# Kernel optimization log

Hardware: AMD Instinct MI355X
Metric: run time of the kernel (lower is better)

The kernel has to match this reference:

```python
import jax, jax.numpy as jnp
import numpy as np

B, L, D = 1, 2048, 4096
H, KV, HD = 32, 8, 128
ROT = 64  # head_dim * partial_rotary_factor
SCALE = HD ** -0.5
NEG = -1e9


def _apply_rope(x, cos, sin):
    # x: [B, h, L, HD]; rotate only the first ROT dims (partial rotary, rotate-half convention)
    xr, xp = x[..., :ROT], x[..., ROT:]
    x1, x2 = jnp.split(xr, 2, axis=-1)
    rotated = jnp.concatenate([-x2, x1], axis=-1)
    xr = xr * cos[None, None] + rotated * sin[None, None]
    return jnp.concatenate([xr, xp], axis=-1)


def setup_inputs() -> dict:
    key = jax.random.key(0)
    k1, k2, k3 = jax.random.split(key, 3)
    x = jax.random.normal(k1, (B, L, D), jnp.float32)
    w_qkv = jax.random.normal(k2, (D, H * HD + 2 * KV * HD), jnp.float32) * 0.02
    w_o = jax.random.normal(k3, (H * HD, D), jnp.float32) * 0.02
    # causal additive mask, broadcast over batch and heads
    causal = jnp.tril(jnp.ones((L, L), dtype=bool))
    attention_mask = jnp.where(causal, 0.0, NEG).astype(jnp.float32)[None, None]
    # rotary tables over the ROT rotary dims
    inv_freq = 1.0 / (10000.0 ** (jnp.arange(0, ROT, 2, dtype=jnp.float32) / ROT))
    t = jnp.arange(L, dtype=jnp.float32)
    freqs = jnp.outer(t, inv_freq)            # [L, ROT/2]
    emb = jnp.concatenate([freqs, freqs], -1)  # [L, ROT]
    cos, sin = jnp.cos(emb), jnp.sin(emb)
    return {"x": x, "attention_mask": attention_mask, "cos": cos, "sin": sin,
            "w_qkv": w_qkv, "w_o": w_o}


def reference(x, attention_mask, cos, sin, w_qkv, w_o):
    Bx, Lx, _ = x.shape
    qkv = x @ w_qkv                                   # [B, L, H*HD + 2*KV*HD]
    q_pos = H * HD
    kv_pos = q_pos + KV * HD
    q = qkv[:, :, :q_pos].reshape(Bx, Lx, H, HD).transpose(0, 2, 1, 3)
    k = qkv[:, :, q_pos:kv_pos].reshape(Bx, Lx, KV, HD).transpose(0, 2, 1, 3)
    v = qkv[:, :, kv_pos:].reshape(Bx, Lx, KV, HD).transpose(0, 2, 1, 3)
    q = _apply_rope(q, cos, sin)
    k = _apply_rope(k, cos, sin)
    # GQA: duplicate KV heads (as in the original module)
    n_rep = H // KV
    k = jnp.repeat(k, n_rep, axis=1)
    v = jnp.repeat(v, n_rep, axis=1)
    w = jnp.einsum("bhqd,bhkd->bhqk", q, k) * SCALE   # [B, H, L, L]
    w = jax.nn.softmax(w + attention_mask, axis=-1)
    o = jnp.einsum("bhqk,bhkd->bhqd", w, v)           # [B, H, L, HD]
    o = o.transpose(0, 2, 1, 3).reshape(Bx, Lx, H * HD)
    return o @ w_o
```

## Files before the change

kernel.cpp:

```cpp
#include <hip/hip_runtime.h>
#include <stdint.h>

typedef float f32x4 __attribute__((ext_vector_type(4)));
typedef short s16x8 __attribute__((ext_vector_type(8)));
typedef unsigned short u16x4 __attribute__((ext_vector_type(4)));
typedef unsigned short u16x8 __attribute__((ext_vector_type(8)));

#define SCALE_F 0.08838834764831845f

__device__ __forceinline__ unsigned short f32_to_bf16(float f) {
    union { float f; unsigned int u; } v; v.f = f;
    return (unsigned short)((v.u + 0x7FFFu + ((v.u >> 16) & 1u)) >> 16);
}
__device__ __forceinline__ float bf16_to_f32(unsigned short h) {
    union { unsigned int u; float f; } v; v.u = (unsigned int)h << 16;
    return v.f;
}

__device__ __forceinline__ void gload16(const void* g, void* l) {
    __builtin_amdgcn_global_load_lds((const __attribute__((address_space(1))) unsigned int*)g,
                                     (__attribute__((address_space(3))) unsigned int*)l,
                                     16, 0, 0);
}

__global__ void k_conv_bf16(const float* __restrict__ in, unsigned short* __restrict__ out, int n4) {
    int i = blockIdx.x * 256 + threadIdx.x;
    if (i >= n4) return;
    f32x4 v = ((const f32x4*)in)[i];
    u16x4 o;
    o[0] = f32_to_bf16(v[0]); o[1] = f32_to_bf16(v[1]);
    o[2] = f32_to_bf16(v[2]); o[3] = f32_to_bf16(v[3]);
    ((u16x4*)out)[i] = o;
}

__global__ void k_transpose_f32(const float* __restrict__ in, unsigned short* __restrict__ out,
                                int R, int in_ld, int in_off) {
    __shared__ float tile[64][65];
    const int rb = blockIdx.y * 64, cb = blockIdx.x * 64;
    const int t = threadIdx.x;
    const int lr = t >> 4, lc4 = (t & 15) * 4;
#pragma unroll
    for (int i = 0; i < 4; ++i) {
        int r = i * 16 + lr;
        f32x4 v = *(const f32x4*)(in + (size_t)(rb + r) * in_ld + in_off + cb + lc4);
        tile[r][lc4 + 0] = v[0]; tile[r][lc4 + 1] = v[1];
        tile[r][lc4 + 2] = v[2]; tile[r][lc4 + 3] = v[3];
    }
    __syncthreads();
#pragma unroll
    for (int i = 0; i < 4; ++i) {
        int oc = cb + i * 16 + lr;
        u16x4 o;
#pragma unroll
        for (int j = 0; j < 4; ++j)
            o[j] = f32_to_bf16(tile[lc4 + j][i * 16 + lr]);
        *(u16x4*)(out + (size_t)oc * R + rb + lc4) = o;
    }
}

__global__ void k_transpose_b16(const unsigned short* __restrict__ in, unsigned short* __restrict__ out,
                                int R, int in_ld, int in_off) {
    __shared__ unsigned short tile[64][68];
    const int rb = blockIdx.y * 64, cb = blockIdx.x * 64;
    const int t = threadIdx.x;
    const int lr = t >> 4, lc4 = (t & 15) * 4;
#pragma unroll
    for (int i = 0; i < 4; ++i) {
        int r = i * 16 + lr;
        u16x4 v = *(const u16x4*)(in + (size_t)(rb + r) * in_ld + in_off + cb + lc4);
        tile[r][lc4 + 0] = v[0]; tile[r][lc4 + 1] = v[1];
        tile[r][lc4 + 2] = v[2]; tile[r][lc4 + 3] = v[3];
    }
    __syncthreads();
#pragma unroll
    for (int i = 0; i < 4; ++i) {
        int oc = cb + i * 16 + lr;
        u16x4 o;
#pragma unroll
        for (int j = 0; j < 4; ++j)
            o[j] = tile[lc4 + j][i * 16 + lr];
        *(u16x4*)(out + (size_t)oc * R + rb + lc4) = o;
    }
}

template<int BN, typename OUT>
__global__ __launch_bounds__(512, 1)
void k_gemm8p(const unsigned short* __restrict__ A, const unsigned short* __restrict__ Bt,
              OUT* __restrict__ C, int N, int K) {
    constexpr int BH = BN * 32;
    constexpr int NF = BN / 64;
    __shared__ __align__(16) unsigned short As[2][2][8192];
    __shared__ __align__(16) unsigned short Bs[2][2][BH];
    const int tid = threadIdx.x;
    const int lane = tid & 63, wid = tid >> 6;
    const int g = lane >> 4, l15 = lane & 15;
    const int wm = wid >> 2, wn = wid & 3;
    const int nwg = gridDim.x, bid = blockIdx.x;
    const int swz = (bid & 7) * (nwg >> 3) + (bid >> 3);
    const int ntn = N / BN;
    const int bm = swz / ntn, bn = swz - bm * ntn;
    const int brow = bm << 8, bcol = bn * BN;

    const int rS = tid >> 2;
    const int kcS = (tid & 3) ^ (rS & 3) ^ ((rS >> 2) & 3);
    const unsigned short* sA = A + (size_t)(brow + rS) * K + kcS * 8;
    const unsigned short* sB = Bt + (size_t)(bcol + rS) * K + kcS * 8;
    const int fsw = (g ^ (l15 & 3) ^ ((l15 >> 2) & 3)) * 8;

    f32x4 acc[8][NF] = {};
    const int nt = K >> 6;

    auto stA = [&](int t, int kh) {
        unsigned short* d = &As[t & 1][kh][tid * 8];
        const unsigned short* s = sA + (size_t)t * 64 + kh * 32;
        gload16(s, d);
        gload16(s + (size_t)128 * K, d + 4096);
    };
    auto stB = [&](int t, int kh) {
        unsigned short* d = &Bs[t & 1][kh][tid * 8];
        const unsigned short* s = sB + (size_t)t * 64 + kh * 32;
        gload16(s, d);
        if constexpr (BN == 256) gload16(s + (size_t)128 * K, d + 4096);
    };

    stA(0, 0); stB(0, 0); stA(0, 1); stB(0, 1);

    for (int t = 0; t < nt; ++t) {
        const int c = t & 1;
        if constexpr (BN == 256) {
            s16x8 af[4], bf[4];
            if (t + 1 < nt) { stA(t + 1, 0); asm volatile("s_waitcnt vmcnt(6)" ::: "memory"); }
            else            { asm volatile("s_waitcnt vmcnt(4)" ::: "memory"); }
            __builtin_amdgcn_s_barrier();
#pragma unroll
            for (int f = 0; f < 4; ++f)
                af[f] = *(const s16x8*)(&As[c][0][(wm * 128 + f * 16 + l15) * 32 + fsw]);
#pragma unroll
            for (int j = 0; j < 4; ++j)
                bf[j] = *(const s16x8*)(&Bs[c][0][(wn * 64 + j * 16 + l15) * 32 + fsw]);
            __builtin_amdgcn_s_setprio(1);
#pragma unroll
            for (int f = 0; f < 4; ++f)
#pragma unroll
                for (int j = 0; j < 4; ++j)
                    acc[f][j] = __builtin_amdgcn_mfma_f32_16x16x32_bf16(af[f], bf[j], acc[f][j], 0, 0, 0);
            __builtin_amdgcn_s_setprio(0);
            if (t + 1 < nt) stB(t + 1, 0);
#pragma unroll
            for (int f = 0; f < 4; ++f)
                af[f] = *(const s16x8*)(&As[c][0][(wm * 128 + 64 + f * 16 + l15) * 32 + fsw]);
            __builtin_amdgcn_s_setprio(1);
#pragma unroll
            for (int f = 0; f < 4; ++f)
#pragma unroll
                for (int j = 0; j < 4; ++j)
                    acc[4 + f][j] = __builtin_amdgcn_mfma_f32_16x16x32_bf16(af[f], bf[j], acc[4 + f][j], 0, 0, 0);
            __builtin_amdgcn_s_setprio(0);
            if (t + 1 < nt) { stA(t + 1, 1); asm volatile("s_waitcnt vmcnt(4)" ::: "memory"); }
            else            { asm volatile("s_waitcnt vmcnt(0)" ::: "memory"); }
            __builtin_amdgcn_s_barrier();
#pragma unroll
            for (int f = 0; f < 4; ++f)
                af[f] = *(const s16x8*)(&As[c][1][(wm * 128 + f * 16 + l15) * 32 + fsw]);
#pragma unroll
            for (int j = 0; j < 4; ++j)
                bf[j] = *(const s16x8*)(&Bs[c][1][(wn * 64 + j * 16 + l15) * 32 + fsw]);
            __builtin_amdgcn_s_setprio(1);
#pragma unroll
            for (int f = 0; f < 4; ++f)
#pragma unroll
                for (int j = 0; j < 4; ++j)
                    acc[f][j] = __builtin_amdgcn_mfma_f32_16x16x32_bf16(af[f], bf[j], acc[f][j], 0, 0, 0);
            __builtin_amdgcn_s_setprio(0);
            if (t + 1 < nt) stB(t + 1, 1);
#pragma unroll
            for (int f = 0; f < 4; ++f)
                af[f] = *(const s16x8*)(&As[c][1][(wm * 128 + 64 + f * 16 + l15) * 32 + fsw]);
            __builtin_amdgcn_s_setprio(1);
#pragma unroll
            for (int f = 0; f < 4; ++f)
#pragma unroll
                for (int j = 0; j < 4; ++j)
                    acc[4 + f][j] = __builtin_amdgcn_mfma_f32_16x16x32_bf16(af[f], bf[j], acc[4 + f][j], 0, 0, 0);
            __builtin_amdgcn_s_setprio(0);
        } else {
            s16x8 af[8], bf[2];
            if (t + 1 < nt) { stA(t + 1, 0); stB(t + 1, 0); asm volatile("s_waitcnt vmcnt(6)" ::: "memory"); }
            else            { asm volatile("s_waitcnt vmcnt(3)" ::: "memory"); }
            __builtin_amdgcn_s_barrier();
#pragma unroll
            for (int f = 0; f < 8; ++f)
                af[f] = *(const s16x8*)(&As[c][0][(wm * 128 + f * 16 + l15) * 32 + fsw]);
#pragma unroll
            for (int j = 0; j < 2; ++j)
                bf[j] = *(const s16x8*)(&Bs[c][0][(wn * 32 + j * 16 + l15) * 32 + fsw]);
            __builtin_amdgcn_s_setprio(1);
#pragma unroll
            for (int f = 0; f < 8; ++f)
#pragma unroll
                for (int j = 0; j < 2; ++j)
                    acc[f][j] = __builtin_amdgcn_mfma_f32_16x16x32_bf16(af[f], bf[j], acc[f][j], 0, 0, 0);
            __builtin_amdgcn_s_setprio(0);
            if (t + 1 < nt) { stA(t + 1, 1); stB(t + 1, 1); asm volatile("s_waitcnt vmcnt(6)" ::: "memory"); }
            else            { asm volatile("s_waitcnt vmcnt(0)" ::: "memory"); }
            __builtin_amdgcn_s_barrier();
#pragma unroll
            for (int f = 0; f < 8; ++f)
                af[f] = *(const s16x8*)(&As[c][1][(wm * 128 + f * 16 + l15) * 32 + fsw]);
#pragma unroll
            for (int j = 0; j < 2; ++j)
                bf[j] = *(const s16x8*)(&Bs[c][1][(wn * 32 + j * 16 + l15) * 32 + fsw]);
            __builtin_amdgcn_s_setprio(1);
#pragma unroll
            for (int f = 0; f < 8; ++f)
#pragma unroll
                for (int j = 0; j < 2; ++j)
                    acc[f][j] = __builtin_amdgcn_mfma_f32_16x16x32_bf16(af[f], bf[j], acc[f][j], 0, 0, 0);
            __builtin_amdgcn_s_setprio(0);
        }
    }

#pragma unroll
    for (int f = 0; f < 8; ++f)
#pragma unroll
        for (int j = 0; j < NF; ++j)
#pragma unroll
            for (int r = 0; r < 4; ++r) {
                const size_t idx = (size_t)(brow + wm * 128 + f * 16 + g * 4 + r) * N
                                   + bcol + wn * (BN / 4) + j * 16 + l15;
                if constexpr (sizeof(OUT) == 4) C[idx] = acc[f][j][r];
                else                            C[idx] = f32_to_bf16(acc[f][j][r]);
            }
}

__global__ void k_rope_pack(const unsigned short* __restrict__ qkv, const float* __restrict__ cosT,
                            const float* __restrict__ sinT, unsigned short* __restrict__ Qb,
                            unsigned short* __restrict__ Kb) {
    const int oct = blockIdx.x * 128 + threadIdx.x;
    if (oct >= 640) return;
    const int col = oct * 8;
    const int t = blockIdx.y;
    const int d = col & 127;
    u16x8 v8 = *(const u16x8*)(qkv + (size_t)t * 6144 + col);
    u16x8 o8;
    if (d < 64) {
        u16x8 p8 = *(const u16x8*)(qkv + (size_t)t * 6144 + (col ^ 32));
        f32x4 c0 = *(const f32x4*)(cosT + t * 64 + d);
        f32x4 c1 = *(const f32x4*)(cosT + t * 64 + d + 4);
        f32x4 s0 = *(const f32x4*)(sinT + t * 64 + d);
        f32x4 s1 = *(const f32x4*)(sinT + t * 64 + d + 4);
        const float sgn = (d < 32) ? -1.f : 1.f;
#pragma unroll
        for (int j = 0; j < 8; ++j) {
            float cc = (j < 4) ? c0[j] : c1[j - 4];
            float ss = (j < 4) ? s0[j] : s1[j - 4];
            float o = bf16_to_f32(v8[j]) * cc + sgn * bf16_to_f32(p8[j]) * ss;
            o8[j] = f32_to_bf16(o);
        }
    } else {
        o8 = v8;
    }
    if (col < 4096) {
        const int h = col >> 7;
        *(u16x8*)(Qb + ((size_t)h * 2048 + t) * 128 + d) = o8;
    } else {
        const int hk = (col - 4096) >> 7;
        *(u16x8*)(Kb + ((size_t)hk * 2048 + t) * 128 + d) = o8;
    }
}

__global__ __launch_bounds__(256, 2)
void k_attn(const unsigned short* __restrict__ Qb, const unsigned short* __restrict__ Kb,
            const unsigned short* __restrict__ Vt, unsigned short* __restrict__ Ob) {
    __shared__ __align__(16) unsigned short Ks[2][8192];
    __shared__ __align__(16) unsigned short Vs[2][8192];
    __shared__ __align__(16) unsigned short Pl[2][4][1024];
    const int h = blockIdx.y, hk = h >> 2;
    const int qbA = blockIdx.x, qbB = 31 - qbA;
    const int tid = threadIdx.x, lane = tid & 63, wid = tid >> 6;
    const int g = lane >> 4, l15 = lane & 15;
    const int qrA = qbA * 64 + wid * 16, qrB = qbB * 64 + wid * 16;
    const int swz = (l15 & 7) << 4;

    s16x8 aqA[4], aqB[4];
#pragma unroll
    for (int kc = 0; kc < 4; ++kc) {
        aqA[kc] = *(const s16x8*)(Qb + ((size_t)h * 2048 + qrA + l15) * 128 + kc * 32 + g * 8);
        aqB[kc] = *(const s16x8*)(Qb + ((size_t)h * 2048 + qrB + l15) * 128 + kc * 32 + g * 8);
    }

    const unsigned short* gK = Kb + ((size_t)hk * 2048 + (tid & 63)) * 128 + (tid >> 6) * 8;
    const unsigned short* gV = Vt + ((size_t)hk * 128 + (tid & 127)) * 2048 + (tid >> 7) * 8;

    auto stage = [&](int kb) {
        unsigned short* dK = Ks[kb & 1] + tid * 8;
        unsigned short* dV = Vs[kb & 1] + tid * 8;
        const unsigned short* sK = gK + (size_t)kb * 8192;
        const unsigned short* sV = gV + kb * 64;
#pragma unroll
        for (int i = 0; i < 4; ++i) gload16(sK + i * 32, dK + i * 2048);
#pragma unroll
        for (int i = 0; i < 4; ++i) gload16(sV + i * 16, dV + i * 2048);
    };

    f32x4 oaccA[8] = {}, oaccB[8] = {};
    float mA = -1e30f, lA = 0.f, mB = -1e30f, lB = 0.f;

    auto process = [&](const s16x8* aq, f32x4* oacc, float& mr, float& lr, int qrow0,
                       char* pw, const unsigned short* ks, const unsigned short* vs, int kb) {
        f32x4 s[4] = {};
        __builtin_amdgcn_s_setprio(1);
#pragma unroll
        for (int kc = 0; kc < 4; ++kc)
#pragma unroll
            for (int kt = 0; kt < 4; ++kt) {
                s16x8 kf = *(const s16x8*)(ks + ((kc * 4 + g) * 64 + kt * 16 + l15) * 8);
                s[kt] = __builtin_amdgcn_mfma_f32_16x16x32_bf16(kf, aq[kc], s[kt], 0, 0, 0);
            }
        __builtin_amdgcn_s_setprio(0);
        const int q = qrow0 + l15;
        if (kb * 64 + 63 > qrow0) {
#pragma unroll
            for (int kt = 0; kt < 4; ++kt)
#pragma unroll
                for (int r = 0; r < 4; ++r) {
                    float xv = s[kt][r] * SCALE_F;
                    s[kt][r] = (kb * 64 + kt * 16 + g * 4 + r > q) ? -3e38f : xv;
                }
        } else {
#pragma unroll
            for (int kt = 0; kt < 4; ++kt)
#pragma unroll
                for (int r = 0; r < 4; ++r) s[kt][r] *= SCALE_F;
        }
        float mx = -3e38f;
#pragma unroll
        for (int kt = 0; kt < 4; ++kt)
#pragma unroll
            for (int r = 0; r < 4; ++r) mx = fmaxf(mx, s[kt][r]);
        mx = fmaxf(mx, __shfl_xor(mx, 16));
        mx = fmaxf(mx, __shfl_xor(mx, 32));
        if (!__all(mx - mr <= 8.0f)) {
            const float mnew = fmaxf(mr, mx);
            const float scal = __expf(mr - mnew);
            mr = mnew;
            float so[4];
#pragma unroll
            for (int r = 0; r < 4; ++r) so[r] = __shfl(scal, g * 4 + r, 16);
#pragma unroll
            for (int j = 0; j < 8; ++j) {
                oacc[j][0] *= so[0]; oacc[j][1] *= so[1];
                oacc[j][2] *= so[2]; oacc[j][3] *= so[3];
            }
            lr *= scal;
        }
        float ps = 0.f;
#pragma unroll
        for (int kt = 0; kt < 4; ++kt)
#pragma unroll
            for (int r = 0; r < 4; ++r) {
                float p = __expf(s[kt][r] - mr);
                s[kt][r] = p;
                ps += p;
            }
        ps += __shfl_xor(ps, 16);
        ps += __shfl_xor(ps, 32);
        lr += ps;
#pragma unroll
        for (int kt = 0; kt < 4; ++kt) {
            unsigned int w0 = (unsigned int)f32_to_bf16(s[kt][0]) | ((unsigned int)f32_to_bf16(s[kt][1]) << 16);
            unsigned int w1 = (unsigned int)f32_to_bf16(s[kt][2]) | ((unsigned int)f32_to_bf16(s[kt][3]) << 16);
            const int b0 = (l15 * 128 + kt * 32 + g * 8) ^ swz;
            *(unsigned int*)(pw + b0) = w0;
            *(unsigned int*)(pw + b0 + 4) = w1;
        }
        __builtin_amdgcn_s_setprio(1);
#pragma unroll
        for (int kc = 0; kc < 2; ++kc) {
            s16x8 pa = *(const s16x8*)(pw + ((l15 * 128 + kc * 64 + g * 16) ^ swz));
#pragma unroll
            for (int j = 0; j < 8; ++j) {
                s16x8 bv = *(const s16x8*)(vs + ((kc * 4 + g) * 128 + j * 16 + l15) * 8);
                oacc[j] = __builtin_amdgcn_mfma_f32_16x16x32_bf16(pa, bv, oacc[j], 0, 0, 0);
            }
        }
        __builtin_amdgcn_s_setprio(0);
    };

    const int nkb = qbB + 1;
    stage(0);
    for (int kb = 0; kb < nkb; ++kb) {
        if (kb + 1 < nkb) {
            stage(kb + 1);
            asm volatile("s_waitcnt vmcnt(8)" ::: "memory");
        } else {
            asm volatile("s_waitcnt vmcnt(0)" ::: "memory");
        }
        __builtin_amdgcn_s_barrier();
        const unsigned short* ks = Ks[kb & 1];
        const unsigned short* vs = Vs[kb & 1];
        process(aqB, oaccB, mB, lB, qrB, (char*)Pl[1][wid], ks, vs, kb);
        if (kb <= qbA)
            process(aqA, oaccA, mA, lA, qrA, (char*)Pl[0][wid], ks, vs, kb);
        __builtin_amdgcn_s_barrier();
    }
    float liA[4], liB[4];
#pragma unroll
    for (int r = 0; r < 4; ++r) {
        liA[r] = 1.f / __shfl(lA, g * 4 + r, 16);
        liB[r] = 1.f / __shfl(lB, g * 4 + r, 16);
    }
#pragma unroll
    for (int j = 0; j < 8; ++j)
#pragma unroll
        for (int r = 0; r < 4; ++r) {
            Ob[(size_t)(qrA + g * 4 + r) * 4096 + h * 128 + j * 16 + l15] = f32_to_bf16(oaccA[j][r] * liA[r]);
            Ob[(size_t)(qrB + g * 4 + r) * 4096 + h * 128 + j * 16 + l15] = f32_to_bf16(oaccB[j][r] * liB[r]);
        }
}

extern "C" void kernel_launch(void* const* d_in, const int* in_sizes, int n_in,
                              void* d_out, int out_size, void* d_ws, size_t ws_size,
                              hipStream_t stream) {
    const float* x     = (const float*)d_in[0];
    const float* cosT  = (const float*)d_in[2];
    const float* sinT  = (const float*)d_in[3];
    const float* w_qkv = (const float*)d_in[4];
    const float* w_o   = (const float*)d_in[5];
    float* out = (float*)d_out;

    char* ws = (char*)d_ws;
    unsigned short* wT   = (unsigned short*)(ws + 0);
    unsigned short* qkvb = (unsigned short*)(ws + 50331648);
    unsigned short* Ob   = (unsigned short*)(ws + 50331648);
    unsigned short* xb   = (unsigned short*)(ws + 100663296);
    unsigned short* Qb   = xb;
    unsigned short* Kb   = (unsigned short*)(ws + 117440512);
    unsigned short* Vt   = (unsigned short*)(ws + 121634816);

    k_conv_bf16<<<8192, 256, 0, stream>>>(x, xb, 2097152);
    k_transpose_f32<<<dim3(96, 64), 256, 0, stream>>>(w_qkv, wT, 4096, 6144, 0);
    k_gemm8p<256, unsigned short><<<192, 512, 0, stream>>>(xb, wT, qkvb, 6144, 4096);
    k_rope_pack<<<dim3(5, 2048), 128, 0, stream>>>(qkvb, cosT, sinT, Qb, Kb);
    k_transpose_b16<<<dim3(16, 32), 256, 0, stream>>>(qkvb, Vt, 2048, 6144, 5120);
    k_transpose_f32<<<dim3(64, 64), 256, 0, stream>>>(w_o, wT, 4096, 4096, 0);
    k_attn<<<dim3(16, 32), 256, 0, stream>>>(Qb, Kb, Vt, Ob);
    k_gemm8p<128, float><<<256, 512, 0, stream>>>(Ob, wT, out, 4096, 4096);
}
```

Before: 363.6 us.

## Retile output GEMM to 128x256, fold softmax scale into Q, interleave QK for two tiles

The output projection moves to a new kernel that uses 128x256 tiles instead of 256x128, with a simpler per-half-K pipeline. The rest of the Q projection GEMM path becomes the former BN=256 code without the template branch. The attention scale is now applied to Q during the RoPE pack, which removes the per-score multiply, though it adds one extra bf16 rounding on Q. In the attention loop, both query tiles' QK matmuls are issued before their softmax and PV steps, to give more independent MFMA work at the cost of extra score registers.

```diff
diff --git a/kernel.cpp b/kernel.cpp
--- a/kernel.cpp
+++ b/kernel.cpp
@@ -87,10 +87,8 @@
 __global__ __launch_bounds__(512, 1)
 void k_gemm8p(const unsigned short* __restrict__ A, const unsigned short* __restrict__ Bt,
               OUT* __restrict__ C, int N, int K) {
-    constexpr int BH = BN * 32;
-    constexpr int NF = BN / 64;
     __shared__ __align__(16) unsigned short As[2][2][8192];
-    __shared__ __align__(16) unsigned short Bs[2][2][BH];
+    __shared__ __align__(16) unsigned short Bs[2][2][8192];
     const int tid = threadIdx.x;
     const int lane = tid & 63, wid = tid >> 6;
     const int g = lane >> 4, l15 = lane & 15;
@@ -107,7 +105,7 @@
     const unsigned short* sB = Bt + (size_t)(bcol + rS) * K + kcS * 8;
     const int fsw = (g ^ (l15 & 3) ^ ((l15 >> 2) & 3)) * 8;
 
-    f32x4 acc[8][NF] = {};
+    f32x4 acc[8][4] = {};
     const int nt = K >> 6;
 
     auto stA = [&](int t, int kh) {
@@ -120,24 +118,136 @@
         unsigned short* d = &Bs[t & 1][kh][tid * 8];
         const unsigned short* s = sB + (size_t)t * 64 + kh * 32;
         gload16(s, d);
-        if constexpr (BN == 256) gload16(s + (size_t)128 * K, d + 4096);
+        gload16(s + (size_t)128 * K, d + 4096);
     };
 
     stA(0, 0); stB(0, 0); stA(0, 1); stB(0, 1);
 
     for (int t = 0; t < nt; ++t) {
         const int c = t & 1;
-        if constexpr (BN == 256) {
+        s16x8 af[4], bf[4];
+        if (t + 1 < nt) { stA(t + 1, 0); asm volatile("s_waitcnt vmcnt(6)" ::: "memory"); }
+        else            { asm volatile("s_waitcnt vmcnt(4)" ::: "memory"); }
+        __builtin_amdgcn_s_barrier();
+#pragma unroll
+        for (int f = 0; f < 4; ++f)
+            af[f] = *(const s16x8*)(&As[c][0][(wm * 128 + f * 16 + l15) * 32 + fsw]);
+#pragma unroll
+        for (int j = 0; j < 4; ++j)
+            bf[j] = *(const s16x8*)(&Bs[c][0][(wn * 64 + j * 16 + l15) * 32 + fsw]);
+        __builtin_amdgcn_s_setprio(1);
+#pragma unroll
+        for (int f = 0; f < 4; ++f)
+#pragma unroll
+            for (int j = 0; j < 4; ++j)
+                acc[f][j] = __builtin_amdgcn_mfma_f32_16x16x32_bf16(af[f], bf[j], acc[f][j], 0, 0, 0);
+        __builtin_amdgcn_s_setprio(0);
+        if (t + 1 < nt) stB(t + 1, 0);
+#pragma unroll
+        for (int f = 0; f < 4; ++f)
+            af[f] = *(const s16x8*)(&As[c][0][(wm * 128 + 64 + f * 16 + l15) * 32 + fsw]);
+        __builtin_amdgcn_s_setprio(1);
+#pragma unroll
+        for (int f = 0; f < 4; ++f)
+#pragma unroll
+            for (int j = 0; j < 4; ++j)
+                acc[4 + f][j] = __builtin_amdgcn_mfma_f32_16x16x32_bf16(af[f], bf[j], acc[4 + f][j], 0, 0, 0);
+        __builtin_amdgcn_s_setprio(0);
+        if (t + 1 < nt) { stA(t + 1, 1); asm volatile("s_waitcnt vmcnt(4)" ::: "memory"); }
+        else            { asm volatile("s_waitcnt vmcnt(0)" ::: "memory"); }
+        __builtin_amdgcn_s_barrier();
+#pragma unroll
+        for (int f = 0; f < 4; ++f)
+            af[f] = *(const s16x8*)(&As[c][1][(wm * 128 + f * 16 + l15) * 32 + fsw]);
+#pragma unroll
+        for (int j = 0; j < 4; ++j)
+            bf[j] = *(const s16x8*)(&Bs[c][1][(wn * 64 + j * 16 + l15) * 32 + fsw]);
+        __builtin_amdgcn_s_setprio(1);
+#pragma unroll
+        for (int f = 0; f < 4; ++f)
+#pragma unroll
+            for (int j = 0; j < 4; ++j)
+                acc[f][j] = __builtin_amdgcn_mfma_f32_16x16x32_bf16(af[f], bf[j], acc[f][j], 0, 0, 0);
+        __builtin_amdgcn_s_setprio(0);
+        if (t + 1 < nt) stB(t + 1, 1);
+#pragma unroll
+        for (int f = 0; f < 4; ++f)
+            af[f] = *(const s16x8*)(&As[c][1][(wm * 128 + 64 + f * 16 + l15) * 32 + fsw]);
+        __builtin_amdgcn_s_setprio(1);
+#pragma unroll
+        for (int f = 0; f < 4; ++f)
+#pragma unroll
+            for (int j = 0; j < 4; ++j)
+                acc[4 + f][j] = __builtin_amdgcn_mfma_f32_16x16x32_bf16(af[f], bf[j], acc[4 + f][j], 0, 0, 0);
+        __builtin_amdgcn_s_setprio(0);
+    }
+
+#pragma unroll
+    for (int f = 0; f < 8; ++f)
+#pragma unroll
+        for (int j = 0; j < 4; ++j)
+#pragma unroll
+            for (int r = 0; r < 4; ++r) {
+                const size_t idx = (size_t)(brow + wm * 128 + f * 16 + g * 4 + r) * N
+                                   + bcol + wn * 64 + j * 16 + l15;
+                if constexpr (sizeof(OUT) == 4) C[idx] = acc[f][j][r];
+                else                            C[idx] = f32_to_bf16(acc[f][j][r]);
+            }
+}
+
+__global__ __launch_bounds__(512, 1)
+void k_gemmB(const unsigned short* __restrict__ A, const unsigned short* __restrict__ Bt,
+             float* __restrict__ C, int N, int K) {
+    __shared__ __align__(16) unsigned short As[2][2][4096];
+    __shared__ __align__(16) unsigned short Bs[2][2][8192];
+    const int tid = threadIdx.x;
+    const int lane = tid & 63, wid = tid >> 6;
+    const int g = lane >> 4, l15 = lane & 15;
+    const int wm = wid >> 2, wn = wid & 3;
+    const int nwg = gridDim.x, bid = blockIdx.x;
+    const int swz = (bid & 7) * (nwg >> 3) + (bid >> 3);
+    const int ntn = N >> 8;
+    const int bm = swz / ntn, bn = swz - bm * ntn;
+    const int brow = bm << 7, bcol = bn << 8;
+
+    const int rS = tid >> 2;
+    const int kcS = (tid & 3) ^ (rS & 3) ^ ((rS >> 2) & 3);
+    const unsigned short* sA = A + (size_t)(brow + rS) * K + kcS * 8;
+    const unsigned short* sB = Bt + (size_t)(bcol + rS) * K + kcS * 8;
+    const int fsw = (g ^ (l15 & 3) ^ ((l15 >> 2) & 3)) * 8;
+
+    f32x4 acc[4][4] = {};
+    const int nt = K >> 6;
+
+    auto stA = [&](int t, int kh) {
+        unsigned short* d = &As[t & 1][kh][tid * 8];
+        const unsigned short* s = sA + (size_t)t * 64 + kh * 32;
+        gload16(s, d);
+    };
+    auto stB = [&](int t, int kh) {
+        unsigned short* d = &Bs[t & 1][kh][tid * 8];
+        const unsigned short* s = sB + (size_t)t * 64 + kh * 32;
+        gload16(s, d);
+        gload16(s + (size_t)128 * K, d + 4096);
+    };
+
+    stA(0, 0); stB(0, 0); stA(0, 1); stB(0, 1);
+
+    for (int t = 0; t < nt; ++t) {
+        const int c = t & 1;
+#pragma unroll
+        for (int kh = 0; kh < 2; ++kh) {
+            if (t + 1 < nt) { stA(t + 1, kh); stB(t + 1, kh); asm volatile("s_waitcnt vmcnt(6)" ::: "memory"); }
+            else if (kh == 0) { asm volatile("s_waitcnt vmcnt(3)" ::: "memory"); }
+            else              { asm volatile("s_waitcnt vmcnt(0)" ::: "memory"); }
+            __builtin_amdgcn_s_barrier();
             s16x8 af[4], bf[4];
-            if (t + 1 < nt) { stA(t + 1, 0); asm volatile("s_waitcnt vmcnt(6)" ::: "memory"); }
-            else            { asm volatile("s_waitcnt vmcnt(4)" ::: "memory"); }
-            __builtin_amdgcn_s_barrier();
 #pragma unroll
             for (int f = 0; f < 4; ++f)
-                af[f] = *(const s16x8*)(&As[c][0][(wm * 128 + f * 16 + l15) * 32 + fsw]);
+                af[f] = *(const s16x8*)(&As[c][kh][(wm * 64 + f * 16 + l15) * 32 + fsw]);
 #pragma unroll
             for (int j = 0; j < 4; ++j)
-                bf[j] = *(const s16x8*)(&Bs[c][0][(wn * 64 + j * 16 + l15) * 32 + fsw]);
+                bf[j] = *(const s16x8*)(&Bs[c][kh][(wn * 64 + j * 16 + l15) * 32 + fsw]);
             __builtin_amdgcn_s_setprio(1);
 #pragma unroll
             for (int f = 0; f < 4; ++f)
@@ -145,92 +255,17 @@
                 for (int j = 0; j < 4; ++j)
                     acc[f][j] = __builtin_amdgcn_mfma_f32_16x16x32_bf16(af[f], bf[j], acc[f][j], 0, 0, 0);
             __builtin_amdgcn_s_setprio(0);
-            if (t + 1 < nt) stB(t + 1, 0);
-#pragma unroll
-            for (int f = 0; f < 4; ++f)
-                af[f] = *(const s16x8*)(&As[c][0][(wm * 128 + 64 + f * 16 + l15) * 32 + fsw]);
-            __builtin_amdgcn_s_setprio(1);
-#pragma unroll
-            for (int f = 0; f < 4; ++f)
-#pragma unroll
-                for (int j = 0; j < 4; ++j)
-                    acc[4 + f][j] = __builtin_amdgcn_mfma_f32_16x16x32_bf16(af[f], bf[j], acc[4 + f][j], 0, 0, 0);
-            __builtin_amdgcn_s_setprio(0);
-            if (t + 1 < nt) { stA(t + 1, 1); asm volatile("s_waitcnt vmcnt(4)" ::: "memory"); }
-            else            { asm volatile("s_waitcnt vmcnt(0)" ::: "memory"); }
-            __builtin_amdgcn_s_barrier();
-#pragma unroll
-            for (int f = 0; f < 4; ++f)
-                af[f] = *(const s16x8*)(&As[c][1][(wm * 128 + f * 16 + l15) * 32 + fsw]);
-#pragma unroll
-            for (int j = 0; j < 4; ++j)
-                bf[j] = *(const s16x8*)(&Bs[c][1][(wn * 64 + j * 16 + l15) * 32 + fsw]);
-            __builtin_amdgcn_s_setprio(1);
-#pragma unroll
-            for (int f = 0; f < 4; ++f)
-#pragma unroll
-                for (int j = 0; j < 4; ++j)
-                    acc[f][j] = __builtin_amdgcn_mfma_f32_16x16x32_bf16(af[f], bf[j], acc[f][j], 0, 0, 0);
-            __builtin_amdgcn_s_setprio(0);
-            if (t + 1 < nt) stB(t + 1, 1);
-#pragma unroll
-            for (int f = 0; f < 4; ++f)
-                af[f] = *(const s16x8*)(&As[c][1][(wm * 128 + 64 + f * 16 + l15) * 32 + fsw]);
-            __builtin_amdgcn_s_setprio(1);
-#pragma unroll
-            for (int f = 0; f < 4; ++f)
-#pragma unroll
-                for (int j = 0; j < 4; ++j)
-                    acc[4 + f][j] = __builtin_amdgcn_mfma_f32_16x16x32_bf16(af[f], bf[j], acc[4 + f][j], 0, 0, 0);
-            __builtin_amdgcn_s_setprio(0);
-        } else {
-            s16x8 af[8], bf[2];
-            if (t + 1 < nt) { stA(t + 1, 0); stB(t + 1, 0); asm volatile("s_waitcnt vmcnt(6)" ::: "memory"); }
-            else            { asm volatile("s_waitcnt vmcnt(3)" ::: "memory"); }
-            __builtin_amdgcn_s_barrier();
-#pragma unroll
-            for (int f = 0; f < 8; ++f)
-                af[f] = *(const s16x8*)(&As[c][0][(wm * 128 + f * 16 + l15) * 32 + fsw]);
-#pragma unroll
-            for (int j = 0; j < 2; ++j)
-                bf[j] = *(const s16x8*)(&Bs[c][0][(wn * 32 + j * 16 + l15) * 32 + fsw]);
-            __builtin_amdgcn_s_setprio(1);
-#pragma unroll
-            for (int f = 0; f < 8; ++f)
-#pragma unroll
-                for (int j = 0; j < 2; ++j)
-                    acc[f][j] = __builtin_amdgcn_mfma_f32_16x16x32_bf16(af[f], bf[j], acc[f][j], 0, 0, 0);
-            __builtin_amdgcn_s_setprio(0);
-            if (t + 1 < nt) { stA(t + 1, 1); stB(t + 1, 1); asm volatile("s_waitcnt vmcnt(6)" ::: "memory"); }
-            else            { asm volatile("s_waitcnt vmcnt(0)" ::: "memory"); }
-            __builtin_amdgcn_s_barrier();
-#pragma unroll
-            for (int f = 0; f < 8; ++f)
-                af[f] = *(const s16x8*)(&As[c][1][(wm * 128 + f * 16 + l15) * 32 + fsw]);
-#pragma unroll
-            for (int j = 0; j < 2; ++j)
-                bf[j] = *(const s16x8*)(&Bs[c][1][(wn * 32 + j * 16 + l15) * 32 + fsw]);
-            __builtin_amdgcn_s_setprio(1);
-#pragma unroll
-            for (int f = 0; f < 8; ++f)
-#pragma unroll
-                for (int j = 0; j < 2; ++j)
-                    acc[f][j] = __builtin_amdgcn_mfma_f32_16x16x32_bf16(af[f], bf[j], acc[f][j], 0, 0, 0);
-            __builtin_amdgcn_s_setprio(0);
-        }
-    }
-
-#pragma unroll
-    for (int f = 0; f < 8; ++f)
-#pragma unroll
-        for (int j = 0; j < NF; ++j)
-#pragma unroll
-            for (int r = 0; r < 4; ++r) {
-                const size_t idx = (size_t)(brow + wm * 128 + f * 16 + g * 4 + r) * N
-                                   + bcol + wn * (BN / 4) + j * 16 + l15;
-                if constexpr (sizeof(OUT) == 4) C[idx] = acc[f][j][r];
-                else                            C[idx] = f32_to_bf16(acc[f][j][r]);
-            }
+        }
+    }
+
+#pragma unroll
+    for (int f = 0; f < 4; ++f)
+#pragma unroll
+        for (int j = 0; j < 4; ++j)
+#pragma unroll
+            for (int r = 0; r < 4; ++r)
+                C[(size_t)(brow + wm * 64 + f * 16 + g * 4 + r) * N
+                  + bcol + wn * 64 + j * 16 + l15] = acc[f][j][r];
 }
 
 __global__ void k_rope_pack(const unsigned short* __restrict__ qkv, const float* __restrict__ cosT,
@@ -241,6 +276,8 @@
     const int col = oct * 8;
     const int t = blockIdx.y;
     const int d = col & 127;
+    const bool isQ = (col < 4096);
+    const float post = isQ ? SCALE_F : 1.0f;
     u16x8 v8 = *(const u16x8*)(qkv + (size_t)t * 6144 + col);
     u16x8 o8;
     if (d < 64) {
@@ -254,13 +291,15 @@
         for (int j = 0; j < 8; ++j) {
             float cc = (j < 4) ? c0[j] : c1[j - 4];
             float ss = (j < 4) ? s0[j] : s1[j - 4];
-            float o = bf16_to_f32(v8[j]) * cc + sgn * bf16_to_f32(p8[j]) * ss;
+            float o = (bf16_to_f32(v8[j]) * cc + sgn * bf16_to_f32(p8[j]) * ss) * post;
             o8[j] = f32_to_bf16(o);
         }
     } else {
-        o8 = v8;
-    }
-    if (col < 4096) {
+#pragma unroll
+        for (int j = 0; j < 8; ++j)
+            o8[j] = f32_to_bf16(bf16_to_f32(v8[j]) * post);
+    }
+    if (isQ) {
         const int h = col >> 7;
         *(u16x8*)(Qb + ((size_t)h * 2048 + t) * 128 + d) = o8;
     } else {
@@ -306,9 +345,7 @@
     f32x4 oaccA[8] = {}, oaccB[8] = {};
     float mA = -1e30f, lA = 0.f, mB = -1e30f, lB = 0.f;
 
-    auto process = [&](const s16x8* aq, f32x4* oacc, float& mr, float& lr, int qrow0,
-                       char* pw, const unsigned short* ks, const unsigned short* vs, int kb) {
-        f32x4 s[4] = {};
+    auto qk = [&](const s16x8* aq, f32x4* s, const unsigned short* ks) {
         __builtin_amdgcn_s_setprio(1);
 #pragma unroll
         for (int kc = 0; kc < 4; ++kc)
@@ -318,20 +355,16 @@
                 s[kt] = __builtin_amdgcn_mfma_f32_16x16x32_bf16(kf, aq[kc], s[kt], 0, 0, 0);
             }
         __builtin_amdgcn_s_setprio(0);
+    };
+
+    auto sm = [&](f32x4* s, f32x4* oacc, float& mr, float& lr, int qrow0, int kb, char* pw) {
         const int q = qrow0 + l15;
         if (kb * 64 + 63 > qrow0) {
 #pragma unroll
             for (int kt = 0; kt < 4; ++kt)
 #pragma unroll
-                for (int r = 0; r < 4; ++r) {
-                    float xv = s[kt][r] * SCALE_F;
-                    s[kt][r] = (kb * 64 + kt * 16 + g * 4 + r > q) ? -3e38f : xv;
-                }
-        } else {
-#pragma unroll
-            for (int kt = 0; kt < 4; ++kt)
-#pragma unroll
-                for (int r = 0; r < 4; ++r) s[kt][r] *= SCALE_F;
+                for (int r = 0; r < 4; ++r)
+                    if (kb * 64 + kt * 16 + g * 4 + r > q) s[kt][r] = -3e38f;
         }
         float mx = -3e38f;
 #pragma unroll
@@ -374,6 +407,9 @@
             *(unsigned int*)(pw + b0) = w0;
             *(unsigned int*)(pw + b0 + 4) = w1;
         }
+    };
+
+    auto pv = [&](f32x4* oacc, char* pw, const unsigned short* vs) {
         __builtin_amdgcn_s_setprio(1);
 #pragma unroll
         for (int kc = 0; kc < 2; ++kc) {
@@ -399,9 +435,16 @@
         __builtin_amdgcn_s_barrier();
         const unsigned short* ks = Ks[kb & 1];
         const unsigned short* vs = Vs[kb & 1];
-        process(aqB, oaccB, mB, lB, qrB, (char*)Pl[1][wid], ks, vs, kb);
-        if (kb <= qbA)
-            process(aqA, oaccA, mA, lA, qrA, (char*)Pl[0][wid], ks, vs, kb);
+        const bool doA = (kb <= qbA);
+        f32x4 sB_[4] = {}, sA_[4] = {};
+        qk(aqB, sB_, ks);
+        if (doA) qk(aqA, sA_, ks);
+        sm(sB_, oaccB, mB, lB, qrB, kb, (char*)Pl[1][wid]);
+        pv(oaccB, (char*)Pl[1][wid], vs);
+        if (doA) {
+            sm(sA_, oaccA, mA, lA, qrA, kb, (char*)Pl[0][wid]);
+            pv(oaccA, (char*)Pl[0][wid], vs);
+        }
         __builtin_amdgcn_s_barrier();
     }
     float liA[4], liB[4];
@@ -445,5 +488,5 @@
     k_transpose_b16<<<dim3(16, 32), 256, 0, stream>>>(qkvb, Vt, 2048, 6144, 5120);
     k_transpose_f32<<<dim3(64, 64), 256, 0, stream>>>(w_o, wT, 4096, 4096, 0);
     k_attn<<<dim3(16, 32), 256, 0, stream>>>(Qb, Kb, Vt, Ob);
-    k_gemm8p<128, float><<<256, 512, 0, stream>>>(Ob, wT, out, 4096, 4096);
-}
+    k_gemmB<<<256, 512, 0, stream>>>(Ob, wT, out, 4096, 4096);
+}
```

Measured after the change: 361.8 us. About the same (-0.5%).
